# Kernel optimization log

Hardware: AMD Instinct MI355X
Metric: run time of the kernel (lower is better)

Reference implementation:

```python
import jax, jax.numpy as jnp
import numpy as np

NUM_HEADS = 8

def setup_inputs() -> dict:
    key = jax.random.key(0)
    ks = jax.random.split(key, 12)
    T, B, C, D = 2048, 4, 512, 512
    s = 1.0 / np.sqrt(C)
    return {
        "key_in": jax.random.normal(ks[0], (T, B, C), jnp.float32),
        "value_in": jax.random.normal(ks[1], (T, B, C), jnp.float32),
        "query_in": jax.random.normal(ks[2], (T, B, C), jnp.float32),
        "Wk": jax.random.normal(ks[3], (C, D), jnp.float32) * s,
        "bk": jax.random.normal(ks[4], (D,), jnp.float32) * 0.01,
        "Wv": jax.random.normal(ks[5], (C, D), jnp.float32) * s,
        "bv": jax.random.normal(ks[6], (D,), jnp.float32) * 0.01,
        "Wq": jax.random.normal(ks[7], (C, D), jnp.float32) * s,
        "bq": jax.random.normal(ks[8], (D,), jnp.float32) * 0.01,
        "Wo": jax.random.normal(ks[9], (D, D), jnp.float32) * (1.0 / np.sqrt(D)),
        "bo": jax.random.normal(ks[10], (D,), jnp.float32) * 0.01,
    }

def reference(key_in, value_in, query_in, Wk, bk, Wv, bv, Wq, bq, Wo, bo):
    T, B, C = query_in.shape
    D = Wq.shape[1]
    H = NUM_HEADS
    hd = D // H
    scale = 1.0 / np.sqrt(hd).astype(np.float32)
    # Linear projections on (T, B, C) -> (T, B, D), then the original's
    # row-major view(B, -1, H, hd) followed by transpose(1, 2) -> (B, H, T, hd)
    def proj(x, W, b):
        y = x @ W + b                      # (T, B, D)
        return y.reshape(B, -1, H, hd).transpose(0, 2, 1, 3)  # (B, H, T, hd)
    q = proj(query_in, Wq, bq)
    k = proj(key_in, Wk, bk)
    v = proj(value_in, Wv, bv)
    scores = jnp.einsum("bhqd,bhkd->bhqk", q, k) * scale  # (B, H, T, T)
    attn = jax.nn.softmax(scores, axis=-1)
    x = jnp.einsum("bhqk,bhkd->bhqd", attn, v)            # (B, H, T, hd)
    x = x.transpose(0, 2, 1, 3).reshape(T, B, D)          # matches .view(T, B, d_model)
    return x @ Wo + bo
```

## Files before the change

### kernel.cpp

```cpp
#include <hip/hip_runtime.h>
#include <math.h>

#define MROWS 8192
#define DM    512
#define SEQL  2048
#define HDIM  64

typedef __attribute__((ext_vector_type(4))) float floatx4;
typedef _Float16 half2v __attribute__((ext_vector_type(2)));
typedef _Float16 half4v __attribute__((ext_vector_type(4)));
typedef _Float16 half8v __attribute__((ext_vector_type(8)));

#define CEXP 0.18033688011f

__device__ __forceinline__ void gll16(const void* g, void* l) {
    __builtin_amdgcn_global_load_lds(
        (const __attribute__((address_space(1))) unsigned int*)g,
        (__attribute__((address_space(3))) unsigned int*)l, 16, 0, 0);
}

__device__ __forceinline__ half4v pack4(float a, float b, float c, float d) {
    half2v lo = __builtin_bit_cast(half2v, __builtin_amdgcn_cvt_pkrtz(a, b));
    half2v hi = __builtin_bit_cast(half2v, __builtin_amdgcn_cvt_pkrtz(c, d));
    half4v r;
    r[0] = lo[0]; r[1] = lo[1]; r[2] = hi[0]; r[3] = hi[1];
    return r;
}

__global__ __launch_bounds__(256) void cast3(const float* __restrict__ s0,
                                             const float* __restrict__ s1,
                                             const float* __restrict__ s2,
                                             _Float16* __restrict__ d0,
                                             _Float16* __restrict__ d1,
                                             _Float16* __restrict__ d2) {
    const float* s = blockIdx.z == 0 ? s0 : (blockIdx.z == 1 ? s1 : s2);
    _Float16* d = blockIdx.z == 0 ? d0 : (blockIdx.z == 1 ? d1 : d2);
    const size_t i = ((size_t)blockIdx.x * 256 + threadIdx.x) * 8;
    const float4 f0 = *(const float4*)&s[i];
    const float4 f1 = *(const float4*)&s[i + 4];
    half8v o;
    o[0] = (_Float16)f0.x; o[1] = (_Float16)f0.y; o[2] = (_Float16)f0.z; o[3] = (_Float16)f0.w;
    o[4] = (_Float16)f1.x; o[5] = (_Float16)f1.y; o[6] = (_Float16)f1.z; o[7] = (_Float16)f1.w;
    *(half8v*)&d[i] = o;
}

__global__ __launch_bounds__(256) void transw(const float* __restrict__ w0,
                                              const float* __restrict__ w1,
                                              const float* __restrict__ w2,
                                              const float* __restrict__ w3,
                                              _Float16* __restrict__ t0,
                                              _Float16* __restrict__ t1,
                                              _Float16* __restrict__ t2,
                                              _Float16* __restrict__ t3) {
    __shared__ float tile[32][33];
    const float* W = blockIdx.z == 0 ? w0 : (blockIdx.z == 1 ? w1 : (blockIdx.z == 2 ? w2 : w3));
    _Float16* T = blockIdx.z == 0 ? t0 : (blockIdx.z == 1 ? t1 : (blockIdx.z == 2 ? t2 : t3));
    const float sc = (blockIdx.z == 0) ? CEXP : 1.0f;
    const int tx = threadIdx.x & 31, ty = threadIdx.x >> 5;
    const int x = blockIdx.x * 32 + tx;
    const int y0 = blockIdx.y * 32;
#pragma unroll
    for (int i = 0; i < 4; ++i)
        tile[ty + i * 8][tx] = W[(size_t)(y0 + ty + i * 8) * DM + x];
    __syncthreads();
    const int xo = y0 + tx;
#pragma unroll
    for (int i = 0; i < 4; ++i)
        T[(size_t)(blockIdx.x * 32 + ty + i * 8) * DM + xo] = (_Float16)(tile[tx][ty + i * 8] * sc);
}

__global__ __launch_bounds__(256, 2) void gemm_f16(
        const _Float16* __restrict__ A0, const _Float16* __restrict__ A1, const _Float16* __restrict__ A2,
        const _Float16* __restrict__ B0, const _Float16* __restrict__ B1, const _Float16* __restrict__ B2,
        const float* __restrict__ c0, const float* __restrict__ c1, const float* __restrict__ c2,
        void* __restrict__ o0, void* __restrict__ o1, void* __restrict__ o2,
        int modes, float bscale0) {
    __shared__ _Float16 As[128 * 64];
    __shared__ _Float16 Bs[128 * 64];
    const int z = blockIdx.z;
    const _Float16* A  = z == 0 ? A0 : (z == 1 ? A1 : A2);
    const _Float16* Bt = z == 0 ? B0 : (z == 1 ? B1 : B2);
    const float* bias  = z == 0 ? c0 : (z == 1 ? c1 : c2);
    void* outp         = z == 0 ? o0 : (z == 1 ? o1 : o2);
    const int mode = (modes >> (z * 4)) & 15;
    const float bscale = (z == 0) ? bscale0 : 1.0f;

    const int tid = threadIdx.x;
    const int w = tid >> 6, lane = tid & 63;
    const int l15 = lane & 15, quad = lane >> 4;
    const int wr = w >> 1, wc = w & 1;
    const int n0 = blockIdx.x * 128, m0 = blockIdx.y * 128;

    floatx4 acc[4][4];
#pragma unroll
    for (int i = 0; i < 4; ++i)
#pragma unroll
        for (int j = 0; j < 4; ++j) acc[i][j] = (floatx4){0.f, 0.f, 0.f, 0.f};

    for (int kt = 0; kt < DM / 64; ++kt) {
        __syncthreads();
#pragma unroll
        for (int i = 0; i < 4; ++i) {
            const int c = i * 256 + w * 64 + lane;
            const int row = c >> 3, g = c & 7;
            const int kg = g ^ (row & 7);
            gll16(&A[(size_t)(m0 + row) * DM + kt * 64 + kg * 8], &As[c * 8]);
        }
#pragma unroll
        for (int i = 0; i < 4; ++i) {
            const int c = i * 256 + w * 64 + lane;
            const int row = c >> 3, g = c & 7;
            const int kg = g ^ (row & 7);
            gll16(&Bt[(size_t)(n0 + row) * DM + kt * 64 + kg * 8], &Bs[c * 8]);
        }
        __syncthreads();
#pragma unroll
        for (int ks = 0; ks < 2; ++ks) {
            half8v af[4], bfr[4];
#pragma unroll
            for (int i = 0; i < 4; ++i) {
                const int row = wr * 64 + i * 16 + l15;
                af[i] = *(const half8v*)&As[row * 64 + ((ks * 4 + quad) ^ (row & 7)) * 8];
            }
#pragma unroll
            for (int j = 0; j < 4; ++j) {
                const int row = wc * 64 + j * 16 + l15;
                bfr[j] = *(const half8v*)&Bs[row * 64 + ((ks * 4 + quad) ^ (row & 7)) * 8];
            }
#pragma unroll
            for (int i = 0; i < 4; ++i)
#pragma unroll
                for (int j = 0; j < 4; ++j)
                    acc[i][j] = __builtin_amdgcn_mfma_f32_16x16x32_f16(af[i], bfr[j], acc[i][j], 0, 0, 0);
        }
    }
#pragma unroll
    for (int j = 0; j < 4; ++j) {
        const int col = n0 + wc * 64 + j * 16 + l15;
        const float bv = bias[col] * bscale;
#pragma unroll
        for (int i = 0; i < 4; ++i) {
            const int rb = m0 + wr * 64 + i * 16 + quad * 4;
            if (mode == 2) {
                float* of = (float*)outp;
#pragma unroll
                for (int r = 0; r < 4; ++r)
                    of[(size_t)(rb + r) * DM + col] = acc[i][j][r] + bv;
            } else if (mode == 0) {
                _Float16* oh = (_Float16*)outp;
#pragma unroll
                for (int r = 0; r < 4; ++r)
                    oh[(size_t)(rb + r) * DM + col] = (_Float16)(acc[i][j][r] + bv);
            } else {
                _Float16* oh = (_Float16*)outp;
                const int g = rb >> 11, seq = rb & 2047;
                half4v pv;
#pragma unroll
                for (int r = 0; r < 4; ++r) pv[r] = (_Float16)(acc[i][j][r] + bv);
                *(half4v*)&oh[((size_t)g * DM + col) * SEQL + seq] = pv;
            }
        }
    }
}

__global__ __launch_bounds__(256, 2) void attn_mfma(const _Float16* __restrict__ Q16,
                                                    const _Float16* __restrict__ K16,
                                                    const _Float16* __restrict__ Vt,
                                                    _Float16* __restrict__ O16) {
    __shared__ _Float16 Ks[64 * 64];
    __shared__ _Float16 Vs[64 * 64];

    const int tid  = threadIdx.x;
    const int w    = tid >> 6;
    const int lane = tid & 63;
    const int l15  = lane & 15;
    const int quad = lane >> 4;

    const int pair = blockIdx.y;
    const int grp  = pair >> 3;
    const int h    = pair & 7;
    const int q0   = blockIdx.x * 128;
    const int rQ   = grp * SEQL + q0 + w * 32;
    const int cb   = h * HDIM;

    half8v qf[2][2];
#pragma unroll
    for (int qt = 0; qt < 2; ++qt)
#pragma unroll
        for (int ks = 0; ks < 2; ++ks)
            qf[qt][ks] = *(const half8v*)&Q16[(size_t)(rQ + qt * 16 + l15) * DM + cb + ks * 32 + quad * 8];

    floatx4 oacc[2][4], lacc[2];
#pragma unroll
    for (int qt = 0; qt < 2; ++qt) {
        lacc[qt] = (floatx4){0.f, 0.f, 0.f, 0.f};
#pragma unroll
        for (int dt = 0; dt < 4; ++dt) oacc[qt][dt] = (floatx4){0.f, 0.f, 0.f, 0.f};
    }
    half4v ones;
    ones[0] = (_Float16)1.f; ones[1] = (_Float16)1.f; ones[2] = (_Float16)1.f; ones[3] = (_Float16)1.f;

    for (int kt = 0; kt < SEQL / 64; ++kt) {
        __syncthreads();
#pragma unroll
        for (int i = 0; i < 4; ++i) {
            const int c = i * 256 + w * 64 + lane;
            if (c < 512) {
                const int key = c >> 3, g = c & 7;
                const int dg = g ^ (key & 7);
                gll16(&K16[(size_t)(grp * SEQL + kt * 64 + key) * DM + cb + dg * 8], &Ks[c * 8]);
            } else {
                const int cv = c - 512;
                const int d = cv >> 3, g = cv & 7;
                const int kg = g ^ (d & 7);
                gll16(&Vt[((size_t)grp * DM + cb + d) * SEQL + kt * 64 + kg * 8], &Vs[cv * 8]);
            }
        }
        __syncthreads();

        floatx4 st[4][2];
#pragma unroll
        for (int ktile = 0; ktile < 4; ++ktile) {
            const int key = ktile * 16 + l15;
            const half8v kf0 = *(const half8v*)&Ks[key * 64 + ((0 + quad) ^ (key & 7)) * 8];
            const half8v kf1 = *(const half8v*)&Ks[key * 64 + ((4 + quad) ^ (key & 7)) * 8];
#pragma unroll
            for (int qt = 0; qt < 2; ++qt) {
                floatx4 z = {0.f, 0.f, 0.f, 0.f};
                z = __builtin_amdgcn_mfma_f32_16x16x32_f16(kf0, qf[qt][0], z, 0, 0, 0);
                st[ktile][qt] = __builtin_amdgcn_mfma_f32_16x16x32_f16(kf1, qf[qt][1], z, 0, 0, 0);
            }
        }

        half4v pa[4][2];
#pragma unroll
        for (int ktile = 0; ktile < 4; ++ktile)
#pragma unroll
            for (int qt = 0; qt < 2; ++qt)
                pa[ktile][qt] = pack4(__builtin_amdgcn_exp2f(st[ktile][qt][0]),
                                      __builtin_amdgcn_exp2f(st[ktile][qt][1]),
                                      __builtin_amdgcn_exp2f(st[ktile][qt][2]),
                                      __builtin_amdgcn_exp2f(st[ktile][qt][3]));

#pragma unroll
        for (int qt = 0; qt < 2; ++qt)
#pragma unroll
            for (int ktile = 0; ktile < 4; ++ktile)
                lacc[qt] = __builtin_amdgcn_mfma_f32_16x16x16f16(pa[ktile][qt], ones, lacc[qt], 0, 0, 0);

#pragma unroll
        for (int dt = 0; dt < 4; ++dt) {
            const int d = dt * 16 + l15;
#pragma unroll
            for (int ktile = 0; ktile < 4; ++ktile) {
                const int G = ktile * 2 + (quad >> 1);
                const int slot = G ^ (d & 7);
                const half4v vf = *(const half4v*)&Vs[d * 64 + slot * 8 + (quad & 1) * 4];
#pragma unroll
                for (int qt = 0; qt < 2; ++qt)
                    oacc[qt][dt] = __builtin_amdgcn_mfma_f32_16x16x16f16(pa[ktile][qt], vf, oacc[qt][dt], 0, 0, 0);
            }
        }
    }

#pragma unroll
    for (int qt = 0; qt < 2; ++qt)
#pragma unroll
        for (int r = 0; r < 4; ++r) {
            const float inv = __builtin_amdgcn_rcpf(lacc[qt][r]);
            const size_t rowoff = (size_t)(rQ + qt * 16 + quad * 4 + r) * DM + cb;
#pragma unroll
            for (int dt = 0; dt < 4; ++dt)
                O16[rowoff + dt * 16 + l15] = (_Float16)(oacc[qt][dt][r] * inv);
        }
}

extern "C" void kernel_launch(void* const* d_in, const int* in_sizes, int n_in,
                              void* d_out, int out_size, void* d_ws, size_t ws_size,
                              hipStream_t stream) {
    const float* key_in   = (const float*)d_in[0];
    const float* value_in = (const float*)d_in[1];
    const float* query_in = (const float*)d_in[2];
    const float* Wk = (const float*)d_in[3];
    const float* bk = (const float*)d_in[4];
    const float* Wv = (const float*)d_in[5];
    const float* bv = (const float*)d_in[6];
    const float* Wq = (const float*)d_in[7];
    const float* bq = (const float*)d_in[8];
    const float* Wo = (const float*)d_in[9];
    const float* bo = (const float*)d_in[10];
    float* out = (float*)d_out;

    const size_t MAT = (size_t)MROWS * DM;
    _Float16* Xq16 = (_Float16*)d_ws;
    _Float16* Xk16 = Xq16 + MAT;
    _Float16* Xv16 = Xk16 + MAT;
    _Float16* Q16  = Xv16 + MAT;
    _Float16* K16  = Q16 + MAT;
    _Float16* Vtb  = K16 + MAT;
    _Float16* Wqt  = Vtb + MAT;
    _Float16* Wkt  = Wqt + DM * DM;
    _Float16* Wvt  = Wkt + DM * DM;
    _Float16* Wot  = Wvt + DM * DM;
    _Float16* O16  = Xq16;

    const dim3 blk(256);

    cast3<<<dim3(2048, 1, 3), blk, 0, stream>>>(query_in, key_in, value_in, Xq16, Xk16, Xv16);
    transw<<<dim3(16, 16, 4), blk, 0, stream>>>(Wq, Wk, Wv, Wo, Wqt, Wkt, Wvt, Wot);

    gemm_f16<<<dim3(DM / 128, MROWS / 128, 3), blk, 0, stream>>>(
        Xq16, Xk16, Xv16, Wqt, Wkt, Wvt, bq, bk, bv,
        (void*)Q16, (void*)K16, (void*)Vtb, 0 | (0 << 4) | (1 << 8), CEXP);

    attn_mfma<<<dim3(SEQL / 128, 32), blk, 0, stream>>>(Q16, K16, Vtb, O16);

    gemm_f16<<<dim3(DM / 128, MROWS / 128, 1), blk, 0, stream>>>(
        O16, O16, O16, Wot, Wot, Wot, bo, bo, bo,
        (void*)out, (void*)out, (void*)out, 2, 1.0f);
}
```

Baseline: 208.1 us.

## Double-buffer K/V tiles in attention and shrink GEMM N-tile to 64

The attention kernel now keeps two LDS buffers for the K and V tiles. It prefetches the next tile with global_load_lds while the current one is used for MFMA work, which removes one barrier per iteration and hides load latency. The projection and output GEMMs move from 128x128 to 128x64 tiles, with each wave owning 32 rows, and launch bounds allow 3 blocks per CU. This doubles the block count to fill the CUs better, at the cost of less B-tile reuse per block. The prefetch depends on the async LDS loads being complete at the barrier, so correctness rests on the compiler inserting the right waitcnt.

```diff
diff --git a/kernel.cpp b/kernel.cpp
--- a/kernel.cpp
+++ b/kernel.cpp
@@ -69,14 +69,14 @@
         T[(size_t)(blockIdx.x * 32 + ty + i * 8) * DM + xo] = (_Float16)(tile[tx][ty + i * 8] * sc);
 }
 
-__global__ __launch_bounds__(256, 2) void gemm_f16(
+__global__ __launch_bounds__(256, 3) void gemm_f16(
         const _Float16* __restrict__ A0, const _Float16* __restrict__ A1, const _Float16* __restrict__ A2,
         const _Float16* __restrict__ B0, const _Float16* __restrict__ B1, const _Float16* __restrict__ B2,
         const float* __restrict__ c0, const float* __restrict__ c1, const float* __restrict__ c2,
         void* __restrict__ o0, void* __restrict__ o1, void* __restrict__ o2,
         int modes, float bscale0) {
     __shared__ _Float16 As[128 * 64];
-    __shared__ _Float16 Bs[128 * 64];
+    __shared__ _Float16 Bs[64 * 64];
     const int z = blockIdx.z;
     const _Float16* A  = z == 0 ? A0 : (z == 1 ? A1 : A2);
     const _Float16* Bt = z == 0 ? B0 : (z == 1 ? B1 : B2);
@@ -86,14 +86,13 @@
     const float bscale = (z == 0) ? bscale0 : 1.0f;
 
     const int tid = threadIdx.x;
-    const int w = tid >> 6, lane = tid & 63;
-    const int l15 = lane & 15, quad = lane >> 4;
-    const int wr = w >> 1, wc = w & 1;
-    const int n0 = blockIdx.x * 128, m0 = blockIdx.y * 128;
-
-    floatx4 acc[4][4];
-#pragma unroll
-    for (int i = 0; i < 4; ++i)
+    const int w = tid >> 6;
+    const int l15 = tid & 15, quad = (tid & 63) >> 4;
+    const int n0 = blockIdx.x * 64, m0 = blockIdx.y * 128;
+
+    floatx4 acc[2][4];
+#pragma unroll
+    for (int i = 0; i < 2; ++i)
 #pragma unroll
         for (int j = 0; j < 4; ++j) acc[i][j] = (floatx4){0.f, 0.f, 0.f, 0.f};
 
@@ -101,14 +100,14 @@
         __syncthreads();
 #pragma unroll
         for (int i = 0; i < 4; ++i) {
-            const int c = i * 256 + w * 64 + lane;
+            const int c = i * 256 + tid;
             const int row = c >> 3, g = c & 7;
             const int kg = g ^ (row & 7);
             gll16(&A[(size_t)(m0 + row) * DM + kt * 64 + kg * 8], &As[c * 8]);
         }
 #pragma unroll
-        for (int i = 0; i < 4; ++i) {
-            const int c = i * 256 + w * 64 + lane;
+        for (int i = 0; i < 2; ++i) {
+            const int c = i * 256 + tid;
             const int row = c >> 3, g = c & 7;
             const int kg = g ^ (row & 7);
             gll16(&Bt[(size_t)(n0 + row) * DM + kt * 64 + kg * 8], &Bs[c * 8]);
@@ -116,19 +115,19 @@
         __syncthreads();
 #pragma unroll
         for (int ks = 0; ks < 2; ++ks) {
-            half8v af[4], bfr[4];
-#pragma unroll
-            for (int i = 0; i < 4; ++i) {
-                const int row = wr * 64 + i * 16 + l15;
+            half8v af[2], bfr[4];
+#pragma unroll
+            for (int i = 0; i < 2; ++i) {
+                const int row = w * 32 + i * 16 + l15;
                 af[i] = *(const half8v*)&As[row * 64 + ((ks * 4 + quad) ^ (row & 7)) * 8];
             }
 #pragma unroll
             for (int j = 0; j < 4; ++j) {
-                const int row = wc * 64 + j * 16 + l15;
+                const int row = j * 16 + l15;
                 bfr[j] = *(const half8v*)&Bs[row * 64 + ((ks * 4 + quad) ^ (row & 7)) * 8];
             }
 #pragma unroll
-            for (int i = 0; i < 4; ++i)
+            for (int i = 0; i < 2; ++i)
 #pragma unroll
                 for (int j = 0; j < 4; ++j)
                     acc[i][j] = __builtin_amdgcn_mfma_f32_16x16x32_f16(af[i], bfr[j], acc[i][j], 0, 0, 0);
@@ -136,11 +135,11 @@
     }
 #pragma unroll
     for (int j = 0; j < 4; ++j) {
-        const int col = n0 + wc * 64 + j * 16 + l15;
+        const int col = n0 + j * 16 + l15;
         const float bv = bias[col] * bscale;
 #pragma unroll
-        for (int i = 0; i < 4; ++i) {
-            const int rb = m0 + wr * 64 + i * 16 + quad * 4;
+        for (int i = 0; i < 2; ++i) {
+            const int rb = m0 + w * 32 + i * 16 + quad * 4;
             if (mode == 2) {
                 float* of = (float*)outp;
 #pragma unroll
@@ -167,11 +166,10 @@
                                                     const _Float16* __restrict__ K16,
                                                     const _Float16* __restrict__ Vt,
                                                     _Float16* __restrict__ O16) {
-    __shared__ _Float16 Ks[64 * 64];
-    __shared__ _Float16 Vs[64 * 64];
+    __shared__ _Float16 Ks[2][64 * 64];
+    __shared__ _Float16 Vs[2][64 * 64];
 
     const int tid  = threadIdx.x;
-    const int w    = tid >> 6;
     const int lane = tid & 63;
     const int l15  = lane & 15;
     const int quad = lane >> 4;
@@ -180,8 +178,11 @@
     const int grp  = pair >> 3;
     const int h    = pair & 7;
     const int q0   = blockIdx.x * 128;
-    const int rQ   = grp * SEQL + q0 + w * 32;
+    const int rQ   = grp * SEQL + q0 + (tid >> 6) * 32;
     const int cb   = h * HDIM;
+
+    const _Float16* Kbase = K16 + (size_t)grp * SEQL * DM + cb;
+    const _Float16* Vbase = Vt + (size_t)grp * DM * SEQL + (size_t)cb * SEQL;
 
     half8v qf[2][2];
 #pragma unroll
@@ -200,30 +201,46 @@
     half4v ones;
     ones[0] = (_Float16)1.f; ones[1] = (_Float16)1.f; ones[2] = (_Float16)1.f; ones[3] = (_Float16)1.f;
 
+    const int cK = tid * 2;
+
+#define STAGE(KT, B)                                                            \
+    {                                                                           \
+        _Float16* ksb = &Ks[B][0];                                              \
+        _Float16* vsb = &Vs[B][0];                                              \
+        _Pragma("unroll")                                                       \
+        for (int i_ = 0; i_ < 4; ++i_) {                                        \
+            const int c_ = i_ * 256 + tid;                                      \
+            if (c_ < 512) {                                                     \
+                const int key_ = c_ >> 3, g_ = c_ & 7;                          \
+                const int dg_ = g_ ^ (key_ & 7);                                \
+                gll16(&Kbase[(size_t)((KT) * 64 + key_) * DM + dg_ * 8],        \
+                      &ksb[c_ * 8]);                                            \
+            } else {                                                            \
+                const int cv_ = c_ - 512;                                       \
+                const int d_ = cv_ >> 3, g_ = cv_ & 7;                          \
+                const int kg_ = g_ ^ (d_ & 7);                                  \
+                gll16(&Vbase[(size_t)d_ * SEQL + (KT) * 64 + kg_ * 8],          \
+                      &vsb[cv_ * 8]);                                           \
+            }                                                                   \
+        }                                                                       \
+    }
+
+    STAGE(0, 0)
+
     for (int kt = 0; kt < SEQL / 64; ++kt) {
+        const int cur = kt & 1;
         __syncthreads();
-#pragma unroll
-        for (int i = 0; i < 4; ++i) {
-            const int c = i * 256 + w * 64 + lane;
-            if (c < 512) {
-                const int key = c >> 3, g = c & 7;
-                const int dg = g ^ (key & 7);
-                gll16(&K16[(size_t)(grp * SEQL + kt * 64 + key) * DM + cb + dg * 8], &Ks[c * 8]);
-            } else {
-                const int cv = c - 512;
-                const int d = cv >> 3, g = cv & 7;
-                const int kg = g ^ (d & 7);
-                gll16(&Vt[((size_t)grp * DM + cb + d) * SEQL + kt * 64 + kg * 8], &Vs[cv * 8]);
-            }
-        }
-        __syncthreads();
+        if (kt + 1 < SEQL / 64) STAGE(kt + 1, cur ^ 1)
+
+        const _Float16* ksb = &Ks[cur][0];
+        const _Float16* vsb = &Vs[cur][0];
 
         floatx4 st[4][2];
 #pragma unroll
         for (int ktile = 0; ktile < 4; ++ktile) {
             const int key = ktile * 16 + l15;
-            const half8v kf0 = *(const half8v*)&Ks[key * 64 + ((0 + quad) ^ (key & 7)) * 8];
-            const half8v kf1 = *(const half8v*)&Ks[key * 64 + ((4 + quad) ^ (key & 7)) * 8];
+            const half8v kf0 = *(const half8v*)&ksb[key * 64 + ((0 + quad) ^ (key & 7)) * 8];
+            const half8v kf1 = *(const half8v*)&ksb[key * 64 + ((4 + quad) ^ (key & 7)) * 8];
 #pragma unroll
             for (int qt = 0; qt < 2; ++qt) {
                 floatx4 z = {0.f, 0.f, 0.f, 0.f};
@@ -255,7 +272,7 @@
             for (int ktile = 0; ktile < 4; ++ktile) {
                 const int G = ktile * 2 + (quad >> 1);
                 const int slot = G ^ (d & 7);
-                const half4v vf = *(const half4v*)&Vs[d * 64 + slot * 8 + (quad & 1) * 4];
+                const half4v vf = *(const half4v*)&vsb[d * 64 + slot * 8 + (quad & 1) * 4];
 #pragma unroll
                 for (int qt = 0; qt < 2; ++qt)
                     oacc[qt][dt] = __builtin_amdgcn_mfma_f32_16x16x16f16(pa[ktile][qt], vf, oacc[qt][dt], 0, 0, 0);
@@ -309,13 +326,13 @@
     cast3<<<dim3(2048, 1, 3), blk, 0, stream>>>(query_in, key_in, value_in, Xq16, Xk16, Xv16);
     transw<<<dim3(16, 16, 4), blk, 0, stream>>>(Wq, Wk, Wv, Wo, Wqt, Wkt, Wvt, Wot);
 
-    gemm_f16<<<dim3(DM / 128, MROWS / 128, 3), blk, 0, stream>>>(
+    gemm_f16<<<dim3(DM / 64, MROWS / 128, 3), blk, 0, stream>>>(
         Xq16, Xk16, Xv16, Wqt, Wkt, Wvt, bq, bk, bv,
         (void*)Q16, (void*)K16, (void*)Vtb, 0 | (0 << 4) | (1 << 8), CEXP);
 
     attn_mfma<<<dim3(SEQL / 128, 32), blk, 0, stream>>>(Q16, K16, Vtb, O16);
 
-    gemm_f16<<<dim3(DM / 128, MROWS / 128, 1), blk, 0, stream>>>(
+    gemm_f16<<<dim3(DM / 64, MROWS / 128, 1), blk, 0, stream>>>(
         O16, O16, O16, Wot, Wot, Wot, bo, bo, bo,
         (void*)out, (void*)out, (void*)out, 2, 1.0f);
 }
```

Measured after the change: 206.5 us. Within noise of the previous version (-0.8%).
